# Optimization experiments

Measured on AMD Instinct MI355X. Metric: run time of the kernel, lower is better.

The kernel has to match this reference:

```python
import jax, jax.numpy as jnp
import numpy as np

DIM = 96; K = 3; DIL = 1
UF = K + DIL * (K - 1)   # unfoldSize = 5
PAD = UF // 2            # reflection pad = 2


def conv2d(x, w, b=None, pad=0, dil=1, groups=1):
    y = jax.lax.conv_general_dilated(
        x, w, (1, 1), [(pad, pad), (pad, pad)], rhs_dilation=(dil, dil),
        dimension_numbers=('NCHW', 'OIHW', 'NCHW'), feature_group_count=groups)
    if b is not None:
        y = y + b[None, :, None, None]
    return y


def group_norm(x, s, b, groups, eps=1e-5):
    n, c, h, w = x.shape
    xg = x.reshape(n, groups, -1)
    m = xg.mean(-1, keepdims=True)
    v = xg.var(-1, keepdims=True)
    xg = (xg - m) * jax.lax.rsqrt(v + eps)
    return xg.reshape(n, c, h, w) * s[None, :, None, None] + b[None, :, None, None]


def prelu(x, a):
    return jnp.where(x >= 0, x, a[0] * x)


def setup_inputs() -> dict:
    key = jax.random.key(0)
    ks = jax.random.split(key, 16)
    d = DIM; dq = d // 4
    rn = lambda i, shape, sc: jax.random.normal(ks[i], shape, jnp.float32) * sc
    return {
        'x': jax.random.normal(ks[0], (8, d, 128, 128), jnp.float32),
        'cf_w': rn(1, (d * K * K, d, 1, 1), 0.1),
        'gnf_s': jnp.ones((d * K * K,)), 'gnf_b': jnp.zeros((d * K * K,)),
        'lb1_w': rn(2, (dq, d, 1, 1), 0.1), 'lb1_b': jnp.zeros((dq,)), 'pr1': jnp.full((1,), 0.25),
        'lbd1_w': rn(3, (dq, 1, 3, 3), 0.2), 'lbd1_b': jnp.zeros((dq,)),
        'lb2_w': rn(4, (dq, dq, 1, 1), 0.2), 'lb2_b': jnp.zeros((dq,)), 'pr2': jnp.full((1,), 0.25),
        'lbd2_w': rn(5, (dq, 1, 3, 3), 0.2), 'lbd2_b': jnp.zeros((dq,)),
        'lb3_w': rn(6, (dq, dq, 1, 1), 0.2), 'lb3_b': jnp.zeros((dq,)), 'pr3': jnp.full((1,), 0.25),
        'lbd3_w': rn(7, (dq, 1, 3, 3), 0.2), 'lbd3_b': jnp.zeros((dq,)),
        'lb4_w': rn(8, (dq, dq, 1, 1), 0.2), 'lb4_b': jnp.zeros((dq,)), 'pr4': jnp.full((1,), 0.25),
        'lb5_w': rn(9, (d, dq, 1, 1), 0.2), 'lb5_b': jnp.zeros((d,)),
        'gnh_s': jnp.ones((d,)), 'gnh_b': jnp.zeros((d,)),
        'hb_w': rn(10, (d, d, 3, 3), 0.05), 'hb_b': jnp.zeros((d,)),
        'ff1_w': rn(11, (2 * d, 2 * d, 1, 1), 0.07), 'ff1_b': jnp.zeros((2 * d,)),
        'gnff_s': jnp.ones((2 * d,)), 'gnff_b': jnp.zeros((2 * d,)),
        'ff2_w': rn(12, (d, 2 * d, 1, 1), 0.07), 'ff2_b': jnp.zeros((d,)),
    }


def reference(x, cf_w, gnf_s, gnf_b, lb1_w, lb1_b, pr1, lbd1_w, lbd1_b,
              lb2_w, lb2_b, pr2, lbd2_w, lbd2_b, lb3_w, lb3_b, pr3,
              lbd3_w, lbd3_b, lb4_w, lb4_b, pr4, lb5_w, lb5_b,
              gnh_s, gnh_b, hb_w, hb_b, ff1_w, ff1_b, gnff_s, gnff_b,
              ff2_w, ff2_b):
    n, c, h, w = x.shape
    d = DIM; dq = d // 4
    # --- dynamic filter from global average pool ---
    fi = x.mean((2, 3), keepdims=True)                 # (n, d, 1, 1)
    fw = conv2d(fi, cf_w)                              # (n, d*9, 1, 1)
    fw = group_norm(fw, gnf_s, gnf_b, 4)
    fw = jax.nn.softmax(fw.reshape(n, d, K * K), axis=-1)  # (n, d, 9)
    # --- masked unfold (involution gather): only offsets on the (DIL+1)-stride grid ---
    xp = jnp.pad(x, ((0, 0), (0, 0), (PAD, PAD), (PAD, PAD)), mode='reflect')
    offs = [(i, j) for i in range(0, UF, DIL + 1) for j in range(0, UF, DIL + 1)]
    patches = jnp.stack([xp[:, :, i:i + h, j:j + w] for i, j in offs], axis=2)  # (n,d,9,h,w)
    low = jnp.einsum('nckhw,nck->nchw', patches, fw)
    high = x - low
    # --- low-frequency multi-dilation branch ---
    y = prelu(conv2d(low, lb1_w, lb1_b), pr1)
    y = conv2d(y, lbd1_w, lbd1_b, pad=5, dil=5, groups=dq)
    y = prelu(conv2d(y, lb2_w, lb2_b), pr2)
    y = conv2d(y, lbd2_w, lbd2_b, pad=1, groups=dq)
    y = prelu(conv2d(y, lb3_w, lb3_b), pr3)
    y = conv2d(y, lbd3_w, lbd3_b, pad=3, dil=3, groups=dq)
    y = prelu(conv2d(y, lb4_w, lb4_b), pr4)
    enh_low = conv2d(y, lb5_w, lb5_b)
    # --- high-frequency branch (GN -> LeakyReLU -> 3x3) + residual ---
    hh = group_norm(high, gnh_s, gnh_b, 4)
    hh = jnp.where(hh >= 0, hh, 0.01 * hh)
    enh_high = conv2d(hh, hb_w, hb_b, pad=1) + high
    # --- frequency fusion ---
    f = jnp.concatenate([enh_low, enh_high], axis=1)
    f = conv2d(f, ff1_w, ff1_b)
    f = group_norm(f, gnff_s, gnff_b, 4)
    f = jax.nn.gelu(f, approximate=False)
    return conv2d(f, ff2_w, ff2_b)
```

## Files before the change

kernel.cpp:

```cpp
#include <hip/hip_runtime.h>
#include <math.h>

#define HW 16384
#define WIDTH 128

typedef short bf16x8 __attribute__((ext_vector_type(8)));
typedef float f32x4 __attribute__((ext_vector_type(4)));
typedef unsigned short ushort8 __attribute__((ext_vector_type(8)));
typedef unsigned short ushort4v __attribute__((ext_vector_type(4)));
typedef unsigned short ushort2v __attribute__((ext_vector_type(2)));

__device__ __forceinline__ float wave_sum(float v) {
#pragma unroll
  for (int o = 32; o > 0; o >>= 1) v += __shfl_down(v, o, 64);
  return v;
}

__device__ __forceinline__ unsigned short f2bf(float f) {
  unsigned u = __float_as_uint(f);
  return (unsigned short)((u + 0x7fffu + ((u >> 16) & 1u)) >> 16);
}

__device__ __forceinline__ float bf2f(unsigned short s) {
  return __uint_as_float((unsigned)s << 16);
}

__global__ __launch_bounds__(256) void k_mean(const float* __restrict__ x,
                                              float* __restrict__ fi) {
  __shared__ float sm[4];
  int nc = blockIdx.x;
  const float4* p = (const float4*)(x + (size_t)nc * HW);
  float s = 0.f;
  for (int i = threadIdx.x; i < HW / 4; i += 256) {
    float4 v = p[i];
    s += (v.x + v.y) + (v.z + v.w);
  }
  s = wave_sum(s);
  int wid = threadIdx.x >> 6, lane = threadIdx.x & 63;
  if (!lane) sm[wid] = s;
  __syncthreads();
  if (!threadIdx.x) fi[nc] = (sm[0] + sm[1] + sm[2] + sm[3]) * (1.f / 16384.f);
}

__global__ __launch_bounds__(256) void k_filter(const float* __restrict__ fi,
                                                const float* __restrict__ cf_w,
                                                const float* __restrict__ gnf_s,
                                                const float* __restrict__ gnf_b,
                                                float* __restrict__ filt) {
  int n = blockIdx.x;
  int t = threadIdx.x;
  __shared__ __align__(16) float sfi[96];
  __shared__ float sfw[864];
  __shared__ float gstat[8];
  if (t < 96) sfi[t] = fi[n * 96 + t];
  __syncthreads();
  for (int oc = t; oc < 864; oc += 256) {
    const float4* wr = (const float4*)(cf_w + (size_t)oc * 96);
    const float4* fr = (const float4*)sfi;
    float a = 0.f;
#pragma unroll
    for (int q = 0; q < 24; q++) {
      float4 w4 = wr[q];
      float4 f4 = fr[q];
      a += w4.x * f4.x + w4.y * f4.y + w4.z * f4.z + w4.w * f4.w;
    }
    sfw[oc] = a;
  }
  __syncthreads();
  if (t < 4) {
    float s = 0.f, ss = 0.f;
    for (int i = 0; i < 216; i++) {
      float v = sfw[t * 216 + i];
      s += v;
      ss += v * v;
    }
    float m = s * (1.f / 216.f);
    float var = ss * (1.f / 216.f) - m * m;
    gstat[t * 2] = m;
    gstat[t * 2 + 1] = rsqrtf(var + 1e-5f);
  }
  __syncthreads();
  for (int oc = t; oc < 864; oc += 256) {
    int g = oc / 216;
    sfw[oc] = (sfw[oc] - gstat[g * 2]) * gstat[g * 2 + 1] * gnf_s[oc] + gnf_b[oc];
  }
  __syncthreads();
  if (t < 96) {
    float v[9], mx = -1e30f;
#pragma unroll
    for (int k = 0; k < 9; k++) {
      v[k] = sfw[t * 9 + k];
      mx = fmaxf(mx, v[k]);
    }
    float s = 0.f;
#pragma unroll
    for (int k = 0; k < 9; k++) {
      v[k] = expf(v[k] - mx);
      s += v[k];
    }
    float inv = 1.f / s;
#pragma unroll
    for (int k = 0; k < 9; k++) filt[((size_t)n * 96 + t) * 9 + k] = v[k] * inv;
  }
}

__global__ __launch_bounds__(256) void k_invol(const float* __restrict__ x,
                                               const float* __restrict__ filt,
                                               float* __restrict__ low,
                                               float* __restrict__ high) {
  int nc = blockIdx.y;
  const float* xp = x + (size_t)nc * HW;
  const float* fp = filt + (size_t)nc * 9;
  float f[9];
#pragma unroll
  for (int k = 0; k < 9; k++) f[k] = fp[k];
  int idx = blockIdx.x * 256 + threadIdx.x;
  int y = idx >> 7, xx = idx & 127;
  int ry[3], rx[3];
#pragma unroll
  for (int d = 0; d < 3; d++) {
    int p = y + 2 * d - 2;
    if (p < 0) p = -p;
    if (p > 127) p = 254 - p;
    ry[d] = p;
    int q = xx + 2 * d - 2;
    if (q < 0) q = -q;
    if (q > 127) q = 254 - q;
    rx[d] = q;
  }
  float acc = 0.f;
#pragma unroll
  for (int i = 0; i < 3; i++)
#pragma unroll
    for (int j = 0; j < 3; j++) acc = fmaf(f[i * 3 + j], xp[ry[i] * WIDTH + rx[j]], acc);
  float xv = xp[idx];
  size_t o = (size_t)nc * HW + idx;
  low[o] = acc;
  high[o] = xv - acc;
}

template <int CIN, int COUT, bool PRELU>
__global__ __launch_bounds__(256) void k_conv1x1(const float* __restrict__ in,
                                                 const float* __restrict__ w,
                                                 const float* __restrict__ b,
                                                 const float* __restrict__ pr,
                                                 float* __restrict__ out) {
  int n = blockIdx.y;
  int pix = blockIdx.x * 256 + threadIdx.x;
  const float* ip = in + (size_t)n * CIN * HW + pix;
  float acc[COUT];
#pragma unroll
  for (int o = 0; o < COUT; o++) acc[o] = b[o];
  for (int c = 0; c < CIN; c += 4) {
    float v0 = ip[(size_t)c * HW];
    float v1 = ip[(size_t)(c + 1) * HW];
    float v2 = ip[(size_t)(c + 2) * HW];
    float v3 = ip[(size_t)(c + 3) * HW];
#pragma unroll
    for (int o = 0; o < COUT; o++) {
      float4 wv = *(const float4*)(w + (size_t)o * CIN + c);
      acc[o] = fmaf(v0, wv.x, acc[o]);
      acc[o] = fmaf(v1, wv.y, acc[o]);
      acc[o] = fmaf(v2, wv.z, acc[o]);
      acc[o] = fmaf(v3, wv.w, acc[o]);
    }
  }
  float a = PRELU ? pr[0] : 0.f;
  float* op = out + (size_t)n * COUT * HW + pix;
#pragma unroll
  for (int o = 0; o < COUT; o++) {
    float v = acc[o];
    if (PRELU) v = v >= 0.f ? v : a * v;
    op[(size_t)o * HW] = v;
  }
}

__global__ __launch_bounds__(256) void k_lb5(const float* __restrict__ in,
                                             const float* __restrict__ w,
                                             const float* __restrict__ b,
                                             unsigned short* __restrict__ out) {
  int n = blockIdx.y;
  int pix = blockIdx.x * 256 + threadIdx.x;
  const float* ip = in + (size_t)n * 24 * HW + pix;
  float acc[96];
#pragma unroll
  for (int o = 0; o < 96; o++) acc[o] = b[o];
  for (int c = 0; c < 24; c += 4) {
    float v0 = ip[(size_t)c * HW];
    float v1 = ip[(size_t)(c + 1) * HW];
    float v2 = ip[(size_t)(c + 2) * HW];
    float v3 = ip[(size_t)(c + 3) * HW];
#pragma unroll
    for (int o = 0; o < 96; o++) {
      float4 wv = *(const float4*)(w + (size_t)o * 24 + c);
      acc[o] = fmaf(v0, wv.x, acc[o]);
      acc[o] = fmaf(v1, wv.y, acc[o]);
      acc[o] = fmaf(v2, wv.z, acc[o]);
      acc[o] = fmaf(v3, wv.w, acc[o]);
    }
  }
  unsigned short* op = out + ((size_t)n * HW + pix) * 96;
#pragma unroll
  for (int c8 = 0; c8 < 12; c8++) {
    ushort8 pk;
#pragma unroll
    for (int j = 0; j < 8; j++) pk[j] = f2bf(acc[c8 * 8 + j]);
    *(ushort8*)&op[c8 * 8] = pk;
  }
}

template <int DILA>
__global__ __launch_bounds__(256) void k_dw3x3(const float* __restrict__ in,
                                               const float* __restrict__ w,
                                               const float* __restrict__ b,
                                               float* __restrict__ out) {
  int ncz = blockIdx.y;
  int c = ncz % 24;
  float wt[9];
#pragma unroll
  for (int k = 0; k < 9; k++) wt[k] = w[c * 9 + k];
  float acc = b[c];
  int pix = blockIdx.x * 256 + threadIdx.x;
  int y = pix >> 7, xx = pix & 127;
  const float* ip = in + (size_t)ncz * HW;
#pragma unroll
  for (int i = 0; i < 3; i++) {
    int yy = y + DILA * (i - 1);
    if (yy < 0 || yy >= 128) continue;
#pragma unroll
    for (int j = 0; j < 3; j++) {
      int xj = xx + DILA * (j - 1);
      if (xj < 0 || xj >= 128) continue;
      acc = fmaf(wt[i * 3 + j], ip[yy * WIDTH + xj], acc);
    }
  }
  out[(size_t)ncz * HW + pix] = acc;
}

__global__ __launch_bounds__(256) void k_gnhigh_part(const float* __restrict__ h,
                                                     float* __restrict__ stats) {
  int ng = blockIdx.x;
  const float4* p = (const float4*)(h + (size_t)ng * 393216 + (size_t)blockIdx.y * 49152);
  float s = 0.f, ss = 0.f;
  for (int i = threadIdx.x; i < 12288; i += 256) {
    float4 v = p[i];
    s += (v.x + v.y) + (v.z + v.w);
    ss += (v.x * v.x + v.y * v.y) + (v.z * v.z + v.w * v.w);
  }
  s = wave_sum(s);
  ss = wave_sum(ss);
  __shared__ float sm[8];
  int wid = threadIdx.x >> 6, lane = threadIdx.x & 63;
  if (!lane) {
    sm[wid] = s;
    sm[4 + wid] = ss;
  }
  __syncthreads();
  if (!threadIdx.x) {
    atomicAdd(&stats[ng * 2], sm[0] + sm[1] + sm[2] + sm[3]);
    atomicAdd(&stats[ng * 2 + 1], sm[4] + sm[5] + sm[6] + sm[7]);
  }
}

__global__ void k_gnfin(float* stats, float inv_cnt) {
  int i = threadIdx.x;
  float s = stats[i * 2], ss = stats[i * 2 + 1];
  float m = s * inv_cnt;
  float var = ss * inv_cnt - m * m;
  stats[i * 2] = m;
  stats[i * 2 + 1] = rsqrtf(var + 1e-5f);
}

__global__ __launch_bounds__(256) void k_prep_hn(const float* __restrict__ high,
                                                 const float* __restrict__ hstats,
                                                 const float* __restrict__ gs,
                                                 const float* __restrict__ gb,
                                                 unsigned short* __restrict__ hn) {
  __shared__ unsigned short sm[64 * 104];
  int n = blockIdx.y;
  int px0 = blockIdx.x * 64;
  int t = threadIdx.x;
  int px = t & 63, cg = t >> 6;
  float hm[4], hi[4];
#pragma unroll
  for (int g = 0; g < 4; g++) {
    hm[g] = hstats[(n * 4 + g) * 2];
    hi[g] = hstats[(n * 4 + g) * 2 + 1];
  }
#pragma unroll
  for (int c0 = 0; c0 < 96; c0 += 8) {
    int c = c0 + cg * 2;
    int g = c / 24;
    float v0 = high[((size_t)(n * 96 + c)) * HW + px0 + px];
    float v1 = high[((size_t)(n * 96 + c + 1)) * HW + px0 + px];
    float h0 = (v0 - hm[g]) * hi[g] * gs[c] + gb[c];
    float h1 = (v1 - hm[g]) * hi[g] * gs[c + 1] + gb[c + 1];
    h0 = h0 >= 0.f ? h0 : 0.01f * h0;
    h1 = h1 >= 0.f ? h1 : 0.01f * h1;
    ushort2v p;
    p.x = f2bf(h0);
    p.y = f2bf(h1);
    *(ushort2v*)&sm[px * 104 + c] = p;
  }
  __syncthreads();
#pragma unroll
  for (int k = 0; k < 3; k++) {
    int idx = t + k * 256;
    int p = idx / 12, c8 = idx % 12;
    ushort8 v = *(ushort8*)&sm[p * 104 + c8 * 8];
    *(ushort8*)&hn[((size_t)n * HW + px0 + p) * 96 + c8 * 8] = v;
  }
}

__global__ __launch_bounds__(256) void k_prep_w(const float* __restrict__ w,
                                                unsigned short* __restrict__ wbf) {
  int i = blockIdx.x * 256 + threadIdx.x;
  int tap = i / 9216;
  int r = i - tap * 9216;
  int oc = r / 96, cin = r - oc * 96;
  wbf[i] = f2bf(w[(size_t)(oc * 96 + cin) * 9 + tap]);
}

__global__ __launch_bounds__(256) void k_prep_ffw(const float* __restrict__ w1,
                                                  const float* __restrict__ w2,
                                                  unsigned short* __restrict__ o1,
                                                  unsigned short* __restrict__ o2) {
  int i = blockIdx.x * 256 + threadIdx.x;
  if (i < 36864)
    o1[i] = f2bf(w1[i]);
  else
    o2[i - 36864] = f2bf(w2[i - 36864]);
}

__global__ __launch_bounds__(256) void k_hbconv_mfma(const unsigned short* __restrict__ hn,
                                                     const unsigned short* __restrict__ wbf,
                                                     const float* __restrict__ bias,
                                                     const float* __restrict__ high,
                                                     unsigned short* __restrict__ ehigh) {
  __shared__ __align__(16) unsigned short stile[6 * 34 * 104];
  int t = threadIdx.x;
  int n = blockIdx.z;
  int x0 = blockIdx.x * 32, y0 = blockIdx.y * 4;
  for (int idx = t; idx < 2448; idx += 256) {
    int p = idx / 12, c8 = idx % 12;
    int ly = p / 34, lx = p - ly * 34;
    int gy = y0 + ly - 1, gx = x0 + lx - 1;
    ushort8 v = (ushort8)0;
    if ((unsigned)gy < 128u && (unsigned)gx < 128u)
      v = *(const ushort8*)&hn[((size_t)n * HW + gy * 128 + gx) * 96 + c8 * 8];
    *(ushort8*)&stile[(ly * 34 + lx) * 104 + c8 * 8] = v;
  }
  __syncthreads();
  int wv = t >> 6;
  int lane = t & 63;
  int l15 = lane & 15, l4 = lane >> 4;
  f32x4 acc[6][2];
#pragma unroll
  for (int mf = 0; mf < 6; mf++)
#pragma unroll
    for (int nf = 0; nf < 2; nf++) acc[mf][nf] = (f32x4)0.f;
#pragma unroll 1
  for (int tap = 0; tap < 9; tap++) {
    int ky = tap / 3, kx = tap - ky * 3;
    const unsigned short* wt = wbf + (size_t)tap * 9216;
#pragma unroll
    for (int kk = 0; kk < 3; kk++) {
      bf16x8 a[6], b[2];
#pragma unroll
      for (int mf = 0; mf < 6; mf++)
        a[mf] = *(const bf16x8*)&wt[(mf * 16 + l15) * 96 + kk * 32 + l4 * 8];
#pragma unroll
      for (int nf = 0; nf < 2; nf++) {
        int p = (wv + ky) * 34 + (nf * 16 + l15 + kx);
        b[nf] = *(const bf16x8*)&stile[p * 104 + kk * 32 + l4 * 8];
      }
#pragma unroll
      for (int mf = 0; mf < 6; mf++)
#pragma unroll
        for (int nf = 0; nf < 2; nf++)
          acc[mf][nf] = __builtin_amdgcn_mfma_f32_16x16x32_bf16(a[mf], b[nf], acc[mf][nf], 0, 0, 0);
    }
  }
  int gy = y0 + wv;
  unsigned short* sT = stile;
  __syncthreads();
#pragma unroll
  for (int mf = 0; mf < 6; mf++) {
#pragma unroll
    for (int nf = 0; nf < 2; nf++) {
      int lx = nf * 16 + l15;
      int p = wv * 32 + lx;
      ushort4v pk;
#pragma unroll
      for (int r = 0; r < 4; r++) {
        int oc = mf * 16 + l4 * 4 + r;
        size_t o = ((size_t)(n * 96 + oc)) * HW + gy * 128 + x0 + lx;
        float v = acc[mf][nf][r] + bias[oc] + high[o];
        pk[r] = f2bf(v);
      }
      *(ushort4v*)&sT[p * 104 + mf * 16 + l4 * 4] = pk;
    }
  }
  __syncthreads();
  for (int idx = t; idx < 1536; idx += 256) {
    int p = idx / 12, c8 = idx % 12;
    int py = p >> 5, lx = p & 31;
    size_t gpx = (size_t)n * HW + (y0 + py) * 128 + x0 + lx;
    *(ushort8*)&ehigh[gpx * 96 + c8 * 8] = *(ushort8*)&sT[p * 104 + c8 * 8];
  }
}

__global__ __launch_bounds__(256) void k_ff1_mfma(const unsigned short* __restrict__ elow,
                                                  const unsigned short* __restrict__ ehigh,
                                                  const unsigned short* __restrict__ wbf,
                                                  const float* __restrict__ bias,
                                                  unsigned short* __restrict__ tbf,
                                                  float* __restrict__ ffstats) {
  __shared__ __align__(16) unsigned short sB[64 * 200];
  __shared__ float sred[4][8];
  int t = threadIdx.x;
  size_t pxbase = (size_t)blockIdx.x * 64;
  int n = blockIdx.x >> 8;
  for (int idx = t; idx < 1536; idx += 256) {
    int p = idx / 24, c8 = idx % 24;
    ushort8 v = (c8 < 12) ? *(const ushort8*)&elow[(pxbase + p) * 96 + c8 * 8]
                          : *(const ushort8*)&ehigh[(pxbase + p) * 96 + (c8 - 12) * 8];
    *(ushort8*)&sB[p * 200 + c8 * 8] = v;
  }
  __syncthreads();
  int wv = t >> 6, lane = t & 63, l15 = lane & 15, l4 = lane >> 4;
  f32x4 acc[12];
#pragma unroll
  for (int mf = 0; mf < 12; mf++) acc[mf] = (f32x4)0.f;
  const unsigned short* wp = wbf + l15 * 192 + l4 * 8;
  const unsigned short* bp = &sB[(wv * 16 + l15) * 200 + l4 * 8];
#pragma unroll
  for (int kk = 0; kk < 6; kk++) {
    bf16x8 b = *(const bf16x8*)(bp + kk * 32);
#pragma unroll
    for (int mf = 0; mf < 12; mf++) {
      bf16x8 a = *(const bf16x8*)(wp + mf * 3072 + kk * 32);
      acc[mf] = __builtin_amdgcn_mfma_f32_16x16x32_bf16(a, b, acc[mf], 0, 0, 0);
    }
  }
  float s[4] = {0.f, 0.f, 0.f, 0.f}, ss[4] = {0.f, 0.f, 0.f, 0.f};
#pragma unroll
  for (int mf = 0; mf < 12; mf++) {
    int g = mf / 3;
    ushort4v pk;
#pragma unroll
    for (int r = 0; r < 4; r++) {
      float v = acc[mf][r] + bias[mf * 16 + l4 * 4 + r];
      s[g] += v;
      ss[g] += v * v;
      pk[r] = f2bf(v);
    }
    *(ushort4v*)&sB[(wv * 16 + l15) * 200 + mf * 16 + l4 * 4] = pk;
  }
#pragma unroll
  for (int g = 0; g < 4; g++) {
    s[g] = wave_sum(s[g]);
    ss[g] = wave_sum(ss[g]);
  }
  if (!lane) {
#pragma unroll
    for (int g = 0; g < 4; g++) {
      sred[wv][g] = s[g];
      sred[wv][4 + g] = ss[g];
    }
  }
  __syncthreads();
  for (int idx = t; idx < 1536; idx += 256) {
    int p = idx / 24, c8 = idx % 24;
    *(ushort8*)&tbf[(pxbase + p) * 192 + c8 * 8] = *(ushort8*)&sB[p * 200 + c8 * 8];
  }
  if (t < 8) {
    float tot = sred[0][t] + sred[1][t] + sred[2][t] + sred[3][t];
    atomicAdd(&ffstats[(n * 4 + (t & 3)) * 2 + (t >> 2)], tot);
  }
}

__global__ __launch_bounds__(256) void k_ff2_mfma(const unsigned short* __restrict__ tbf,
                                                  const float* __restrict__ ffstats,
                                                  const float* __restrict__ gs,
                                                  const float* __restrict__ gb,
                                                  const unsigned short* __restrict__ wbf,
                                                  const float* __restrict__ bias,
                                                  float* __restrict__ out) {
  __shared__ __align__(16) unsigned short sB[64 * 200];
  int t = threadIdx.x;
  size_t pxbase = (size_t)blockIdx.x * 64;
  int n = blockIdx.x >> 8;
  float fm[4], fvv[4];
#pragma unroll
  for (int g = 0; g < 4; g++) {
    fm[g] = ffstats[(n * 4 + g) * 2];
    fvv[g] = ffstats[(n * 4 + g) * 2 + 1];
  }
  for (int idx = t; idx < 1536; idx += 256) {
    int p = idx / 24, c8 = idx % 24;
    int c = c8 * 8, g = c / 48;
    ushort8 raw = *(const ushort8*)&tbf[(pxbase + p) * 192 + c];
    ushort8 pk;
#pragma unroll
    for (int j = 0; j < 8; j++) {
      float rv = bf2f(raw[j]);
      float z = (rv - fm[g]) * fvv[g] * gs[c + j] + gb[c + j];
      float gl = 0.5f * z * (1.f + erff(z * 0.70710678118654752f));
      pk[j] = f2bf(gl);
    }
    *(ushort8*)&sB[p * 200 + c] = pk;
  }
  __syncthreads();
  int wv = t >> 6, lane = t & 63, l15 = lane & 15, l4 = lane >> 4;
  f32x4 acc[6];
#pragma unroll
  for (int mf = 0; mf < 6; mf++) acc[mf] = (f32x4)0.f;
  const unsigned short* wp = wbf + l15 * 192 + l4 * 8;
  const unsigned short* bp = &sB[(wv * 16 + l15) * 200 + l4 * 8];
#pragma unroll
  for (int kk = 0; kk < 6; kk++) {
    bf16x8 b = *(const bf16x8*)(bp + kk * 32);
#pragma unroll
    for (int mf = 0; mf < 6; mf++) {
      bf16x8 a = *(const bf16x8*)(wp + mf * 3072 + kk * 32);
      acc[mf] = __builtin_amdgcn_mfma_f32_16x16x32_bf16(a, b, acc[mf], 0, 0, 0);
    }
  }
  int lpx = (blockIdx.x & 255) * 64 + wv * 16 + l15;
#pragma unroll
  for (int mf = 0; mf < 6; mf++) {
#pragma unroll
    for (int r = 0; r < 4; r++) {
      int oc = mf * 16 + l4 * 4 + r;
      out[((size_t)(n * 96 + oc)) * HW + lpx] = acc[mf][r] + bias[oc];
    }
  }
}

extern "C" void kernel_launch(void* const* d_in, const int* in_sizes, int n_in,
                              void* d_out, int out_size, void* d_ws, size_t ws_size,
                              hipStream_t stream) {
  const float* x = (const float*)d_in[0];
  const float* cf_w = (const float*)d_in[1];
  const float* gnf_s = (const float*)d_in[2];
  const float* gnf_b = (const float*)d_in[3];
  const float* lb1_w = (const float*)d_in[4];
  const float* lb1_b = (const float*)d_in[5];
  const float* pr1 = (const float*)d_in[6];
  const float* lbd1_w = (const float*)d_in[7];
  const float* lbd1_b = (const float*)d_in[8];
  const float* lb2_w = (const float*)d_in[9];
  const float* lb2_b = (const float*)d_in[10];
  const float* pr2 = (const float*)d_in[11];
  const float* lbd2_w = (const float*)d_in[12];
  const float* lbd2_b = (const float*)d_in[13];
  const float* lb3_w = (const float*)d_in[14];
  const float* lb3_b = (const float*)d_in[15];
  const float* pr3 = (const float*)d_in[16];
  const float* lbd3_w = (const float*)d_in[17];
  const float* lbd3_b = (const float*)d_in[18];
  const float* lb4_w = (const float*)d_in[19];
  const float* lb4_b = (const float*)d_in[20];
  const float* pr4 = (const float*)d_in[21];
  const float* lb5_w = (const float*)d_in[22];
  const float* lb5_b = (const float*)d_in[23];
  const float* gnh_s = (const float*)d_in[24];
  const float* gnh_b = (const float*)d_in[25];
  const float* hb_w = (const float*)d_in[26];
  const float* hb_b = (const float*)d_in[27];
  const float* ff1_w = (const float*)d_in[28];
  const float* ff1_b = (const float*)d_in[29];
  const float* gnff_s = (const float*)d_in[30];
  const float* gnff_b = (const float*)d_in[31];
  const float* ff2_w = (const float*)d_in[32];
  const float* ff2_b = (const float*)d_in[33];

  const size_t SPC = (size_t)8 * 96 * HW;
  const size_t YSZ = (size_t)8 * 24 * HW;
  float* ws = (float*)d_ws;
  float* buf_low = ws;
  unsigned short* buf_tbf = (unsigned short*)ws;
  float* buf_high = ws + SPC;
  unsigned short* buf_hn = (unsigned short*)(ws + 2 * SPC);
  unsigned short* buf_ehigh = (unsigned short*)(ws + 2 * SPC + SPC / 2);
  unsigned short* buf_elow = (unsigned short*)(ws + 3 * SPC);
  unsigned short* buf_wbf = (unsigned short*)(ws + 3 * SPC + SPC / 2);
  unsigned short* buf_wff1 = buf_wbf + 82944;
  unsigned short* buf_wff2 = buf_wff1 + 36864;
  float* buf_y1 = ws + 4 * SPC;
  float* buf_y2 = buf_y1 + YSZ;
  float* buf_fi = buf_y2 + YSZ;
  float* buf_filt = buf_fi + 768;
  float* buf_hst = buf_filt + 6912;
  float* buf_ffst = buf_hst + 64;

  hipMemsetAsync(buf_hst, 0, 128 * sizeof(float), stream);

  k_mean<<<768, 256, 0, stream>>>(x, buf_fi);
  k_filter<<<8, 256, 0, stream>>>(buf_fi, cf_w, gnf_s, gnf_b, buf_filt);
  k_invol<<<dim3(64, 768), 256, 0, stream>>>(x, buf_filt, buf_low, buf_high);

  k_conv1x1<96, 24, true><<<dim3(64, 8), 256, 0, stream>>>(buf_low, lb1_w, lb1_b, pr1, buf_y1);
  k_dw3x3<5><<<dim3(64, 192), 256, 0, stream>>>(buf_y1, lbd1_w, lbd1_b, buf_y2);
  k_conv1x1<24, 24, true><<<dim3(64, 8), 256, 0, stream>>>(buf_y2, lb2_w, lb2_b, pr2, buf_y1);
  k_dw3x3<1><<<dim3(64, 192), 256, 0, stream>>>(buf_y1, lbd2_w, lbd2_b, buf_y2);
  k_conv1x1<24, 24, true><<<dim3(64, 8), 256, 0, stream>>>(buf_y2, lb3_w, lb3_b, pr3, buf_y1);
  k_dw3x3<3><<<dim3(64, 192), 256, 0, stream>>>(buf_y1, lbd3_w, lbd3_b, buf_y2);
  k_conv1x1<24, 24, true><<<dim3(64, 8), 256, 0, stream>>>(buf_y2, lb4_w, lb4_b, pr4, buf_y1);
  k_lb5<<<dim3(64, 8), 256, 0, stream>>>(buf_y1, lb5_w, lb5_b, buf_elow);

  k_gnhigh_part<<<dim3(32, 8), 256, 0, stream>>>(buf_high, buf_hst);
  k_gnfin<<<1, 32, 0, stream>>>(buf_hst, 1.f / 393216.f);
  k_prep_w<<<324, 256, 0, stream>>>(hb_w, buf_wbf);
  k_prep_ffw<<<216, 256, 0, stream>>>(ff1_w, ff2_w, buf_wff1, buf_wff2);
  k_prep_hn<<<dim3(256, 8), 256, 0, stream>>>(buf_high, buf_hst, gnh_s, gnh_b, buf_hn);
  k_hbconv_mfma<<<dim3(4, 32, 8), 256, 0, stream>>>(buf_hn, buf_wbf, hb_b, buf_high, buf_ehigh);

  k_ff1_mfma<<<2048, 256, 0, stream>>>(buf_elow, buf_ehigh, buf_wff1, ff1_b, buf_tbf, buf_ffst);
  k_gnfin<<<1, 32, 0, stream>>>(buf_ffst, 1.f / 786432.f);
  k_ff2_mfma<<<2048, 256, 0, stream>>>(buf_tbf, buf_ffst, gnff_s, gnff_b, buf_wff2, ff2_b,
                                       (float*)d_out);
}
```

Measured before the change: 707.5 us.

## Fuse depthwise 3x3 into following 1x1 conv and use fast erf GELU

Each depthwise dilated 3x3 conv is now folded into the next 24->24 pointwise conv plus PReLU in one kernel, cutting three launches and three intermediate round trips through global memory. The ff2 kernel's GELU swaps erff for an Abramowitz-Stegun polynomial erf built on rcp and exp, and its staging loads are hoisted so all six vector loads are issued before any math. The polynomial erf carries about 1e-7 absolute error, which is below bf16 rounding. The fused kernel has only 512 blocks, so it loses parallelism compared with the 12288-block depthwise launches.

```diff
diff --git a/kernel.cpp b/kernel.cpp
--- a/kernel.cpp
+++ b/kernel.cpp
@@ -23,6 +23,18 @@
 
 __device__ __forceinline__ float bf2f(unsigned short s) {
   return __uint_as_float((unsigned)s << 16);
+}
+
+__device__ __forceinline__ float gelu_exact(float z) {
+  float u = z * 0.70710678118654752f;
+  float ax = fabsf(u);
+  float t = __builtin_amdgcn_rcpf(fmaf(0.3275911f, ax, 1.0f));
+  float poly = t * fmaf(t, fmaf(t, fmaf(t, fmaf(t, 1.061405429f, -1.453152027f),
+                                        1.421413741f), -0.284496736f), 0.254829592f);
+  float e = __expf(-ax * ax);
+  float erf_abs = fmaf(-poly, e, 1.0f);
+  float erf = copysignf(erf_abs, z);
+  return 0.5f * z * (1.0f + erf);
 }
 
 __global__ __launch_bounds__(256) void k_mean(const float* __restrict__ x,
@@ -175,6 +187,58 @@
   }
 }
 
+template <int DILA>
+__global__ __launch_bounds__(256) void k_dwfuse(const float* __restrict__ in,
+                                                const float* __restrict__ dw,
+                                                const float* __restrict__ dwb,
+                                                const float* __restrict__ w1,
+                                                const float* __restrict__ b1,
+                                                const float* __restrict__ pr,
+                                                float* __restrict__ out) {
+  int n = blockIdx.y;
+  int pix = blockIdx.x * 256 + threadIdx.x;
+  int y = pix >> 7, xx = pix & 127;
+  const float* ip = in + (size_t)n * 24 * HW;
+  float acc[24];
+#pragma unroll
+  for (int o = 0; o < 24; o++) acc[o] = b1[o];
+  for (int c = 0; c < 24; c += 4) {
+    float d[4];
+#pragma unroll
+    for (int q = 0; q < 4; q++) {
+      float a = dwb[c + q];
+      const float* cp = ip + (size_t)(c + q) * HW;
+#pragma unroll
+      for (int i = 0; i < 3; i++) {
+        int yy = y + DILA * (i - 1);
+        if (yy < 0 || yy >= 128) continue;
+#pragma unroll
+        for (int j = 0; j < 3; j++) {
+          int xj = xx + DILA * (j - 1);
+          if (xj < 0 || xj >= 128) continue;
+          a = fmaf(dw[(c + q) * 9 + i * 3 + j], cp[yy * WIDTH + xj], a);
+        }
+      }
+      d[q] = a;
+    }
+#pragma unroll
+    for (int o = 0; o < 24; o++) {
+      float4 wv = *(const float4*)(w1 + (size_t)o * 24 + c);
+      acc[o] = fmaf(d[0], wv.x, acc[o]);
+      acc[o] = fmaf(d[1], wv.y, acc[o]);
+      acc[o] = fmaf(d[2], wv.z, acc[o]);
+      acc[o] = fmaf(d[3], wv.w, acc[o]);
+    }
+  }
+  float a = pr[0];
+  float* op = out + (size_t)n * 24 * HW + pix;
+#pragma unroll
+  for (int o = 0; o < 24; o++) {
+    float v = acc[o];
+    op[(size_t)o * HW] = v >= 0.f ? v : a * v;
+  }
+}
+
 __global__ __launch_bounds__(256) void k_lb5(const float* __restrict__ in,
                                              const float* __restrict__ w,
                                              const float* __restrict__ b,
@@ -207,34 +271,6 @@
     for (int j = 0; j < 8; j++) pk[j] = f2bf(acc[c8 * 8 + j]);
     *(ushort8*)&op[c8 * 8] = pk;
   }
-}
-
-template <int DILA>
-__global__ __launch_bounds__(256) void k_dw3x3(const float* __restrict__ in,
-                                               const float* __restrict__ w,
-                                               const float* __restrict__ b,
-                                               float* __restrict__ out) {
-  int ncz = blockIdx.y;
-  int c = ncz % 24;
-  float wt[9];
-#pragma unroll
-  for (int k = 0; k < 9; k++) wt[k] = w[c * 9 + k];
-  float acc = b[c];
-  int pix = blockIdx.x * 256 + threadIdx.x;
-  int y = pix >> 7, xx = pix & 127;
-  const float* ip = in + (size_t)ncz * HW;
-#pragma unroll
-  for (int i = 0; i < 3; i++) {
-    int yy = y + DILA * (i - 1);
-    if (yy < 0 || yy >= 128) continue;
-#pragma unroll
-    for (int j = 0; j < 3; j++) {
-      int xj = xx + DILA * (j - 1);
-      if (xj < 0 || xj >= 128) continue;
-      acc = fmaf(wt[i * 3 + j], ip[yy * WIDTH + xj], acc);
-    }
-  }
-  out[(size_t)ncz * HW + pix] = acc;
 }
 
 __global__ __launch_bounds__(256) void k_gnhigh_part(const float* __restrict__ h,
@@ -497,19 +533,27 @@
     fm[g] = ffstats[(n * 4 + g) * 2];
     fvv[g] = ffstats[(n * 4 + g) * 2 + 1];
   }
-  for (int idx = t; idx < 1536; idx += 256) {
-    int p = idx / 24, c8 = idx % 24;
-    int c = c8 * 8, g = c / 48;
-    ushort8 raw = *(const ushort8*)&tbf[(pxbase + p) * 192 + c];
+  ushort8 raw[6];
+  int pp[6], cc[6];
+#pragma unroll
+  for (int k = 0; k < 6; k++) {
+    int idx = t + k * 256;
+    int p = idx / 24, c8 = idx - p * 24;
+    pp[k] = p;
+    cc[k] = c8 * 8;
+    raw[k] = *(const ushort8*)&tbf[(pxbase + p) * 192 + cc[k]];
+  }
+#pragma unroll
+  for (int k = 0; k < 6; k++) {
+    int c = cc[k], g = c / 48;
     ushort8 pk;
 #pragma unroll
     for (int j = 0; j < 8; j++) {
-      float rv = bf2f(raw[j]);
+      float rv = bf2f(raw[k][j]);
       float z = (rv - fm[g]) * fvv[g] * gs[c + j] + gb[c + j];
-      float gl = 0.5f * z * (1.f + erff(z * 0.70710678118654752f));
-      pk[j] = f2bf(gl);
-    }
-    *(ushort8*)&sB[p * 200 + c] = pk;
+      pk[j] = f2bf(gelu_exact(z));
+    }
+    *(ushort8*)&sB[pp[k] * 200 + c] = pk;
   }
   __syncthreads();
   int wv = t >> 6, lane = t & 63, l15 = lane & 15, l4 = lane >> 4;
@@ -602,13 +646,13 @@
   k_invol<<<dim3(64, 768), 256, 0, stream>>>(x, buf_filt, buf_low, buf_high);
 
   k_conv1x1<96, 24, true><<<dim3(64, 8), 256, 0, stream>>>(buf_low, lb1_w, lb1_b, pr1, buf_y1);
-  k_dw3x3<5><<<dim3(64, 192), 256, 0, stream>>>(buf_y1, lbd1_w, lbd1_b, buf_y2);
-  k_conv1x1<24, 24, true><<<dim3(64, 8), 256, 0, stream>>>(buf_y2, lb2_w, lb2_b, pr2, buf_y1);
-  k_dw3x3<1><<<dim3(64, 192), 256, 0, stream>>>(buf_y1, lbd2_w, lbd2_b, buf_y2);
-  k_conv1x1<24, 24, true><<<dim3(64, 8), 256, 0, stream>>>(buf_y2, lb3_w, lb3_b, pr3, buf_y1);
-  k_dw3x3<3><<<dim3(64, 192), 256, 0, stream>>>(buf_y1, lbd3_w, lbd3_b, buf_y2);
-  k_conv1x1<24, 24, true><<<dim3(64, 8), 256, 0, stream>>>(buf_y2, lb4_w, lb4_b, pr4, buf_y1);
-  k_lb5<<<dim3(64, 8), 256, 0, stream>>>(buf_y1, lb5_w, lb5_b, buf_elow);
+  k_dwfuse<5><<<dim3(64, 8), 256, 0, stream>>>(buf_y1, lbd1_w, lbd1_b, lb2_w, lb2_b, pr2,
+                                               buf_y2);
+  k_dwfuse<1><<<dim3(64, 8), 256, 0, stream>>>(buf_y2, lbd2_w, lbd2_b, lb3_w, lb3_b, pr3,
+                                               buf_y1);
+  k_dwfuse<3><<<dim3(64, 8), 256, 0, stream>>>(buf_y1, lbd3_w, lbd3_b, lb4_w, lb4_b, pr4,
+                                               buf_y2);
+  k_lb5<<<dim3(64, 8), 256, 0, stream>>>(buf_y2, lb5_w, lb5_b, buf_elow);
 
   k_gnhigh_part<<<dim3(32, 8), 256, 0, stream>>>(buf_high, buf_hst);
   k_gnfin<<<1, 32, 0, stream>>>(buf_hst, 1.f / 393216.f);
```

Result: faster. 689.2 us (-2.6%).
